# Optimization experiments

Measured on AMD Instinct MI355X. Metric: run time of the kernel, lower is better.

Reference implementation:

```python
import jax, jax.numpy as jnp
import numpy as np

ALPHA = 0.2  # LeakyReLU negative slope

def setup_inputs() -> dict:
    key = jax.random.key(0)
    k1, k2, k3, k4 = jax.random.split(key, 4)
    N, F_in, F_out = 8192, 512, 64
    x = jax.random.normal(k1, (N, F_in), dtype=jnp.float32)
    adj = jax.random.randint(k2, (N, N), 0, 2, dtype=jnp.int32)
    # xavier-normal-ish init
    weight = jax.random.normal(k3, (F_in, F_out), dtype=jnp.float32) * np.sqrt(2.0 / (F_in + F_out))
    a = jax.random.normal(k4, (2 * F_out, 1), dtype=jnp.float32) * np.sqrt(2.0 / (2 * F_out + 1))
    return {"x": x, "adj": adj, "weight": weight, "a": a}

def reference(x, adj, weight, a):
    # Wh: [N, F_out]
    Wh = x @ weight
    F_out = weight.shape[1]
    a1 = a[:F_out, 0]   # applies to source (row) node
    a2 = a[F_out:, 0]   # applies to target (col) node
    # e[i,j] = LeakyReLU(Wh[i]@a1 + Wh[j]@a2)  -- broadcast-add instead of O(N^2*2F) concat
    s1 = Wh @ a1        # [N]
    s2 = Wh @ a2        # [N]
    e = s1[:, None] + s2[None, :]              # [N, N]
    e = jnp.where(e > 0, e, ALPHA * e)         # LeakyReLU
    e = jnp.where(adj > 0, e, jnp.float32(-9e15))
    attention = jax.nn.softmax(e, axis=1)      # [N, N]
    h_prime = attention @ Wh                   # [N, F_out]
    return jax.nn.elu(h_prime)                 # concat=True -> ELU
```

## Files before the change

### kernel.cpp

```cpp
#include <hip/hip_runtime.h>
#include <hip/hip_bf16.h>
#include <cstdint>
#include <cstddef>

#define N_NODES 8192
#define F_IN 512
#define F_OUT 64
#define LOG2E 1.44269504f

#define JSPLIT 8
#define JPB (N_NODES / JSPLIT)
#define JC 256
#define NCHUNK (JPB / JC)

typedef __attribute__((ext_vector_type(8))) short short8v;
typedef __attribute__((ext_vector_type(4))) float f32x4;
typedef __attribute__((ext_vector_type(4))) int i32x4;
typedef __attribute__((ext_vector_type(4))) unsigned int u32x4;

static __device__ __forceinline__ unsigned short f2bf(float f) {
    union { float f; unsigned u; } v; v.f = f;
    unsigned u = v.u + 0x7FFFu + ((v.u >> 16) & 1u);
    return (unsigned short)(u >> 16);
}
static __device__ __forceinline__ float bf2f(unsigned short b) {
    union { unsigned u; float f; } v; v.u = ((unsigned)b) << 16;
    return v.f;
}
static __device__ __forceinline__ unsigned cvt_pk_bf16(float lo, float hi) {
    unsigned r;
    asm("v_cvt_pk_bf16_f32 %0, %1, %2" : "=v"(r) : "v"(lo), "v"(hi));
    return r;
}

__global__ __launch_bounds__(256)
void gat_wconv(const float* __restrict__ W, unsigned short* __restrict__ whf,
               unsigned short* __restrict__ wlf) {
    const int t = blockIdx.x * 256 + threadIdx.x;
    const int tile = t >> 6, lane = t & 63;
    const int kt = tile >> 2, ct = tile & 3;
    const int k0 = kt * 32 + ((lane >> 4) << 3);
    const int c  = ct * 16 + (lane & 15);
    short8v h, l;
    #pragma unroll
    for (int i = 0; i < 8; ++i) {
        float v = W[(size_t)(k0 + i) * F_OUT + c];
        unsigned short hb = f2bf(v);
        h[i] = (short)hb;
        l[i] = (short)f2bf(v - bf2f(hb));
    }
    const size_t dst = (size_t)tile * 512 + (size_t)lane * 8;
    *(short8v*)(whf + dst) = h;
    *(short8v*)(wlf + dst) = l;
}

__global__ __launch_bounds__(256)
void gat_prep(const float* __restrict__ x, const unsigned short* __restrict__ whf,
              const unsigned short* __restrict__ wlf, const float* __restrict__ a,
              unsigned short* __restrict__ whtf,
              float* __restrict__ s1, float* __restrict__ s2) {
    __shared__ f32x4 red[2][4][64];
    __shared__ unsigned short ldsT[64][40];
    const int tid = threadIdx.x;
    const int lane = tid & 63;
    const int wv = tid >> 6;
    const int rt = wv & 1;
    const int kh = wv >> 1;
    const int l15 = lane & 15, g = lane >> 4;
    const int jt = blockIdx.x;
    const int row0 = jt * 32 + rt * 16;

    f32x4 acc[4] = {{0.f,0.f,0.f,0.f},{0.f,0.f,0.f,0.f},{0.f,0.f,0.f,0.f},{0.f,0.f,0.f,0.f}};

    const float* xp = x + (size_t)(row0 + l15) * F_IN + kh * 256 + g * 8;
    float4 v[16];
    #pragma unroll
    for (int q = 0; q < 8; ++q) {
        v[2 * q]     = *(const float4*)(xp + q * 32);
        v[2 * q + 1] = *(const float4*)(xp + q * 32 + 4);
    }
    #pragma unroll
    for (int q = 0; q < 8; ++q) {
        const int kt = kh * 8 + q;
        float vv[8] = {v[2*q].x, v[2*q].y, v[2*q].z, v[2*q].w,
                       v[2*q+1].x, v[2*q+1].y, v[2*q+1].z, v[2*q+1].w};
        short8v xh, xl;
        #pragma unroll
        for (int i = 0; i < 8; ++i) {
            unsigned short hb = f2bf(vv[i]);
            xh[i] = (short)hb;
            xl[i] = (short)f2bf(vv[i] - bf2f(hb));
        }
        const unsigned short* wp = whf + (size_t)(kt * 4) * 512 + (size_t)lane * 8;
        const unsigned short* lp = wlf + (size_t)(kt * 4) * 512 + (size_t)lane * 8;
        #pragma unroll
        for (int ct = 0; ct < 4; ++ct) {
            short8v wh = *(const short8v*)(wp + ct * 512);
            short8v wl = *(const short8v*)(lp + ct * 512);
            acc[ct] = __builtin_amdgcn_mfma_f32_16x16x32_bf16(xh, wh, acc[ct], 0, 0, 0);
            acc[ct] = __builtin_amdgcn_mfma_f32_16x16x32_bf16(xl, wh, acc[ct], 0, 0, 0);
            acc[ct] = __builtin_amdgcn_mfma_f32_16x16x32_bf16(xh, wl, acc[ct], 0, 0, 0);
        }
    }

    if (kh == 1) {
        #pragma unroll
        for (int ct = 0; ct < 4; ++ct) red[rt][ct][lane] = acc[ct];
    }
    __syncthreads();

    if (kh == 0) {
        #pragma unroll
        for (int ct = 0; ct < 4; ++ct) acc[ct] += red[rt][ct][lane];

        #pragma unroll
        for (int r = 0; r < 4; ++r) {
            float p1 = 0.f, p2 = 0.f;
            #pragma unroll
            for (int ct = 0; ct < 4; ++ct) {
                p1 = fmaf(acc[ct][r], a[ct * 16 + l15], p1);
                p2 = fmaf(acc[ct][r], a[64 + ct * 16 + l15], p2);
            }
            p1 += __shfl_xor(p1, 1); p2 += __shfl_xor(p2, 1);
            p1 += __shfl_xor(p1, 2); p2 += __shfl_xor(p2, 2);
            p1 += __shfl_xor(p1, 4); p2 += __shfl_xor(p2, 4);
            p1 += __shfl_xor(p1, 8); p2 += __shfl_xor(p2, 8);
            if (l15 == 0) {
                s1[row0 + g * 4 + r] = p1 * LOG2E;
                s2[row0 + g * 4 + r] = p2 * LOG2E;
            }
        }

        #pragma unroll
        for (int ct = 0; ct < 4; ++ct) {
            ushort4 pk;
            pk.x = f2bf(acc[ct][0]); pk.y = f2bf(acc[ct][1]);
            pk.z = f2bf(acc[ct][2]); pk.w = f2bf(acc[ct][3]);
            *(ushort4*)&ldsT[ct * 16 + l15][rt * 16 + g * 4] = pk;
        }
    }
    __syncthreads();

    if (kh == 0) {
        #pragma unroll
        for (int fl = 0; fl < 2; ++fl) {
            const int ft = rt * 2 + fl;
            short8v sv = *(const short8v*)&ldsT[ft * 16 + l15][g * 8];
            *(short8v*)(whtf + ((size_t)jt * 4 + ft) * 512 + (size_t)lane * 8) = sv;
        }
    }
}

__global__ __launch_bounds__(512)
void gat_main(const int* __restrict__ adj, const unsigned short* __restrict__ whtf,
              const float* __restrict__ s1, const float* __restrict__ s2,
              float* __restrict__ numpart, float* __restrict__ denpart) {
    __shared__ unsigned short lds[2][JC * F_OUT];
    const int tid  = threadIdx.x;
    const int lane = tid & 63;
    const int wv   = tid >> 6;
    const int l15  = lane & 15, g = lane >> 4;
    const int rg   = blockIdx.x >> 3;
    const int js   = blockIdx.x & 7;
    const int rowbase = rg * 128 + wv * 16;
    const int row  = rowbase + l15;
    const int j0   = js * JPB;
    const float s1r = s1[row];

    const char* gbase = (const char*)whtf + (size_t)j0 * 128;
    const int*   aprow = adj + (size_t)row * N_NODES + j0 + g * 8;
    const float* s2b   = s2 + j0 + g * 8;

    f32x4 acc0 = {0.f, 0.f, 0.f, 0.f};
    f32x4 acc1 = acc0, acc2 = acc0, acc3 = acc0;
    float dsum = 0.f;

    #define STAGE(ch, buf) do { \
        const char* _g = gbase + (size_t)(ch) * 32768 + (size_t)tid * 16; \
        char* _l = (char*)&lds[buf][0] + (size_t)wv * 1024; \
        _Pragma("unroll") \
        for (int _i = 0; _i < 4; ++_i) \
            __builtin_amdgcn_global_load_lds( \
                (const __attribute__((address_space(1))) void*)(_g + _i * 8192), \
                (__attribute__((address_space(3))) void*)(_l + _i * 8192), 16, 0, 0); \
    } while (0)

    STAGE(0, 0);
    __syncthreads();

    for (int ch = 0; ch < NCHUNK; ++ch) {
        const int cur = ch & 1;
        if (ch < NCHUNK - 1) STAGE(ch + 1, cur ^ 1);

        const unsigned short* lbuf = &lds[cur][0];
        #pragma unroll
        for (int itg = 0; itg < 2; ++itg) {
            i32x4 aj[8];
            #pragma unroll
            for (int q = 0; q < 4; ++q) {
                const i32x4* ap = (const i32x4*)(aprow + ch * JC + itg * 128 + q * 32);
                aj[2 * q]     = ap[0];
                aj[2 * q + 1] = ap[1];
            }
            #pragma unroll
            for (int q = 0; q < 4; ++q) {
                const int it = itg * 4 + q;
                const int jw = ch * JC + it * 32;
                float4 sa = *(const float4*)(s2b + jw);
                float4 sb = *(const float4*)(s2b + jw + 4);

                short8v b0 = *(const short8v*)(lbuf + (it * 4 + 0) * 512 + lane * 8);
                short8v b1 = *(const short8v*)(lbuf + (it * 4 + 1) * 512 + lane * 8);
                short8v b2 = *(const short8v*)(lbuf + (it * 4 + 2) * 512 + lane * 8);
                short8v b3 = *(const short8v*)(lbuf + (it * 4 + 3) * 512 + lane * 8);

                float w0, w1, w2, w3, w4, w5, w6, w7;
                #define GAT_EL(wvar, ajv, s2v) do { \
                    float e = s1r + (s2v); e = fmaxf(e, 0.2f * e); \
                    float ex = __builtin_amdgcn_exp2f(e); \
                    wvar = ((ajv) > 0) ? ex : 0.f; dsum += wvar; } while (0);
                GAT_EL(w0, aj[2*q][0], sa.x) GAT_EL(w1, aj[2*q][1], sa.y)
                GAT_EL(w2, aj[2*q][2], sa.z) GAT_EL(w3, aj[2*q][3], sa.w)
                GAT_EL(w4, aj[2*q+1][0], sb.x) GAT_EL(w5, aj[2*q+1][1], sb.y)
                GAT_EL(w6, aj[2*q+1][2], sb.z) GAT_EL(w7, aj[2*q+1][3], sb.w)
                #undef GAT_EL

                u32x4 au;
                au[0] = cvt_pk_bf16(w0, w1);
                au[1] = cvt_pk_bf16(w2, w3);
                au[2] = cvt_pk_bf16(w4, w5);
                au[3] = cvt_pk_bf16(w6, w7);
                short8v afrag = __builtin_bit_cast(short8v, au);

                acc0 = __builtin_amdgcn_mfma_f32_16x16x32_bf16(afrag, b0, acc0, 0, 0, 0);
                acc1 = __builtin_amdgcn_mfma_f32_16x16x32_bf16(afrag, b1, acc1, 0, 0, 0);
                acc2 = __builtin_amdgcn_mfma_f32_16x16x32_bf16(afrag, b2, acc2, 0, 0, 0);
                acc3 = __builtin_amdgcn_mfma_f32_16x16x32_bf16(afrag, b3, acc3, 0, 0, 0);
            }
        }
        __syncthreads();
    }
    #undef STAGE

    dsum += __shfl_xor(dsum, 16);
    dsum += __shfl_xor(dsum, 32);
    if (lane < 16) denpart[(size_t)js * N_NODES + rowbase + lane] = dsum;

    float* np = numpart + ((size_t)js * N_NODES + rowbase) * F_OUT;
    #pragma unroll
    for (int r = 0; r < 4; ++r) {
        const int ro = (g * 4 + r) * F_OUT;
        np[ro +  0 + l15] = acc0[r];
        np[ro + 16 + l15] = acc1[r];
        np[ro + 32 + l15] = acc2[r];
        np[ro + 48 + l15] = acc3[r];
    }
}

__global__ __launch_bounds__(256)
void gat_combine(const float* __restrict__ numpart, const float* __restrict__ denpart,
                 float* __restrict__ out) {
    const int idx = blockIdx.x * 256 + threadIdx.x;
    const int r = idx >> 6;
    float num = 0.f, den = 0.f;
    #pragma unroll
    for (int c = 0; c < JSPLIT; ++c) {
        num += numpart[(size_t)c * N_NODES * F_OUT + idx];
        den += denpart[(size_t)c * N_NODES + r];
    }
    float h = num / den;
    out[idx] = h > 0.f ? h : __expf(h) - 1.f;
}

extern "C" void kernel_launch(void* const* d_in, const int* in_sizes, int n_in,
                              void* d_out, int out_size, void* d_ws, size_t ws_size,
                              hipStream_t stream) {
    const float* x      = (const float*)d_in[0];
    const int*   adj    = (const int*)d_in[1];
    const float* weight = (const float*)d_in[2];
    const float* a      = (const float*)d_in[3];
    float* out = (float*)d_out;

    char* ws = (char*)d_ws;
    unsigned short* whtf = (unsigned short*)ws;
    float* s1            = (float*)(ws + 1048576);
    float* s2            = (float*)(ws + 1048576 + 32768);
    unsigned short* whf  = (unsigned short*)(ws + 1048576 + 65536);
    unsigned short* wlf  = (unsigned short*)(ws + 1048576 + 131072);
    float* numpart       = (float*)(ws + 1048576 + 196608);
    float* denpart       = (float*)(ws + 1048576 + 196608 + (size_t)JSPLIT * N_NODES * F_OUT * 4);

    gat_wconv<<<16, 256, 0, stream>>>(weight, whf, wlf);
    gat_prep<<<N_NODES / 32, 256, 0, stream>>>(x, whf, wlf, a, whtf, s1, s2);
    gat_main<<<64 * JSPLIT, 512, 0, stream>>>(adj, whtf, s1, s2, numpart, denpart);
    gat_combine<<<N_NODES * F_OUT / 256, 256, 0, stream>>>(numpart, denpart, out);
}
```

Baseline: 85.97 us.

## Remap column-to-K assignment so each lane reads 32 contiguous adjacency ints

Changes which columns each lane group covers inside an MFMA K-slice, so every lane reads a contiguous 128-byte run of adj and s2 instead of strided 32-byte pieces. The Wh^T fragment layout written by the projection kernel is permuted to match, and all threads now take part in the store. It also adds a minimum-blocks hint to launch_bounds on the main kernel. The goal is better global-load coalescing and vector width on the dominant adjacency stream, with some risk of register pressure from the occupancy hint.

```diff
diff --git a/kernel.cpp b/kernel.cpp
--- a/kernel.cpp
+++ b/kernel.cpp
@@ -32,6 +32,7 @@
     asm("v_cvt_pk_bf16_f32 %0, %1, %2" : "=v"(r) : "v"(lo), "v"(hi));
     return r;
 }
+
 
 __global__ __launch_bounds__(256)
 void gat_wconv(const float* __restrict__ W, unsigned short* __restrict__ whf,
@@ -141,17 +142,18 @@
     }
     __syncthreads();
 
-    if (kh == 0) {
-        #pragma unroll
-        for (int fl = 0; fl < 2; ++fl) {
-            const int ft = rt * 2 + fl;
-            short8v sv = *(const short8v*)&ldsT[ft * 16 + l15][g * 8];
-            *(short8v*)(whtf + ((size_t)jt * 4 + ft) * 512 + (size_t)lane * 8) = sv;
-        }
-    }
-}
-
-__global__ __launch_bounds__(512)
+    {
+        const int jb = jt >> 2, gj = jt & 3;
+        const int m  = tid >> 6;
+        const int ct = (tid >> 4) & 3;
+        const int c  = tid & 15;
+        short8v sv = *(const short8v*)&ldsT[ct * 16 + c][m * 8];
+        *(short8v*)(whtf + (size_t)jb * 8192 + m * 2048 + ct * 512
+                         + (size_t)(gj * 16 + c) * 8) = sv;
+    }
+}
+
+__global__ __launch_bounds__(512, 4)
 void gat_main(const int* __restrict__ adj, const unsigned short* __restrict__ whtf,
               const float* __restrict__ s1, const float* __restrict__ s2,
               float* __restrict__ numpart, float* __restrict__ denpart) {
@@ -168,8 +170,8 @@
     const float s1r = s1[row];
 
     const char* gbase = (const char*)whtf + (size_t)j0 * 128;
-    const int*   aprow = adj + (size_t)row * N_NODES + j0 + g * 8;
-    const float* s2b   = s2 + j0 + g * 8;
+    const int*   abase = adj + (size_t)row * N_NODES + j0 + g * 32;
+    const float* s2base = s2 + j0 + g * 32;
 
     f32x4 acc0 = {0.f, 0.f, 0.f, 0.f};
     f32x4 acc1 = acc0, acc2 = acc0, acc3 = acc0;
@@ -194,35 +196,33 @@
 
         const unsigned short* lbuf = &lds[cur][0];
         #pragma unroll
-        for (int itg = 0; itg < 2; ++itg) {
+        for (int jb_l = 0; jb_l < 2; ++jb_l) {
+            const int jg = ch * JC + jb_l * 128;
             i32x4 aj[8];
             #pragma unroll
-            for (int q = 0; q < 4; ++q) {
-                const i32x4* ap = (const i32x4*)(aprow + ch * JC + itg * 128 + q * 32);
-                aj[2 * q]     = ap[0];
-                aj[2 * q + 1] = ap[1];
-            }
+            for (int q = 0; q < 8; ++q)
+                aj[q] = *(const i32x4*)(abase + jg + q * 4);
+
+            const unsigned short* gb = lbuf + jb_l * 8192;
             #pragma unroll
-            for (int q = 0; q < 4; ++q) {
-                const int it = itg * 4 + q;
-                const int jw = ch * JC + it * 32;
-                float4 sa = *(const float4*)(s2b + jw);
-                float4 sb = *(const float4*)(s2b + jw + 4);
-
-                short8v b0 = *(const short8v*)(lbuf + (it * 4 + 0) * 512 + lane * 8);
-                short8v b1 = *(const short8v*)(lbuf + (it * 4 + 1) * 512 + lane * 8);
-                short8v b2 = *(const short8v*)(lbuf + (it * 4 + 2) * 512 + lane * 8);
-                short8v b3 = *(const short8v*)(lbuf + (it * 4 + 3) * 512 + lane * 8);
+            for (int m = 0; m < 4; ++m) {
+                float4 sa = *(const float4*)(s2base + jg + m * 8);
+                float4 sb = *(const float4*)(s2base + jg + m * 8 + 4);
+
+                short8v b0 = *(const short8v*)(gb + m * 2048 +   0 + lane * 8);
+                short8v b1 = *(const short8v*)(gb + m * 2048 + 512 + lane * 8);
+                short8v b2 = *(const short8v*)(gb + m * 2048 + 1024 + lane * 8);
+                short8v b3 = *(const short8v*)(gb + m * 2048 + 1536 + lane * 8);
 
                 float w0, w1, w2, w3, w4, w5, w6, w7;
                 #define GAT_EL(wvar, ajv, s2v) do { \
                     float e = s1r + (s2v); e = fmaxf(e, 0.2f * e); \
                     float ex = __builtin_amdgcn_exp2f(e); \
                     wvar = ((ajv) > 0) ? ex : 0.f; dsum += wvar; } while (0);
-                GAT_EL(w0, aj[2*q][0], sa.x) GAT_EL(w1, aj[2*q][1], sa.y)
-                GAT_EL(w2, aj[2*q][2], sa.z) GAT_EL(w3, aj[2*q][3], sa.w)
-                GAT_EL(w4, aj[2*q+1][0], sb.x) GAT_EL(w5, aj[2*q+1][1], sb.y)
-                GAT_EL(w6, aj[2*q+1][2], sb.z) GAT_EL(w7, aj[2*q+1][3], sb.w)
+                GAT_EL(w0, aj[2*m][0], sa.x) GAT_EL(w1, aj[2*m][1], sa.y)
+                GAT_EL(w2, aj[2*m][2], sa.z) GAT_EL(w3, aj[2*m][3], sa.w)
+                GAT_EL(w4, aj[2*m+1][0], sb.x) GAT_EL(w5, aj[2*m+1][1], sb.y)
+                GAT_EL(w6, aj[2*m+1][2], sb.z) GAT_EL(w7, aj[2*m+1][3], sb.w)
                 #undef GAT_EL
 
                 u32x4 au;
```

Result: slower. 91.07 us (+5.9%).

## Load Wh B-fragments directly from global, drop LDS double buffering

Applied to the files above, without the earlier changes.

Removes the LDS staging of the pre-swizzled Wh tiles and the per-chunk barriers; each wave now reads its MFMA B fragments straight from global memory, which should mostly hit in L2 since every block reads the same data. Launch bounds now request 4 blocks per CU, so the freed LDS and tighter registers allow more resident waves. The cost is more global and L2 traffic for B operands that were previously shared across 8 waves through LDS, and higher load latency that the extra occupancy has to hide.

```diff
diff --git a/kernel.cpp b/kernel.cpp
--- a/kernel.cpp
+++ b/kernel.cpp
@@ -10,8 +10,6 @@
 
 #define JSPLIT 8
 #define JPB (N_NODES / JSPLIT)
-#define JC 256
-#define NCHUNK (JPB / JC)
 
 typedef __attribute__((ext_vector_type(8))) short short8v;
 typedef __attribute__((ext_vector_type(4))) float f32x4;
@@ -151,11 +149,10 @@
     }
 }
 
-__global__ __launch_bounds__(512)
+__global__ __launch_bounds__(512, 4)
 void gat_main(const int* __restrict__ adj, const unsigned short* __restrict__ whtf,
               const float* __restrict__ s1, const float* __restrict__ s2,
               float* __restrict__ numpart, float* __restrict__ denpart) {
-    __shared__ unsigned short lds[2][JC * F_OUT];
     const int tid  = threadIdx.x;
     const int lane = tid & 63;
     const int wv   = tid >> 6;
@@ -167,80 +164,58 @@
     const int j0   = js * JPB;
     const float s1r = s1[row];
 
-    const char* gbase = (const char*)whtf + (size_t)j0 * 128;
     const int*   aprow = adj + (size_t)row * N_NODES + j0 + g * 8;
     const float* s2b   = s2 + j0 + g * 8;
+    const unsigned short* bp = whtf + ((size_t)(j0 >> 5) * 4) * 512 + (size_t)lane * 8;
 
     f32x4 acc0 = {0.f, 0.f, 0.f, 0.f};
     f32x4 acc1 = acc0, acc2 = acc0, acc3 = acc0;
     float dsum = 0.f;
 
-    #define STAGE(ch, buf) do { \
-        const char* _g = gbase + (size_t)(ch) * 32768 + (size_t)tid * 16; \
-        char* _l = (char*)&lds[buf][0] + (size_t)wv * 1024; \
-        _Pragma("unroll") \
-        for (int _i = 0; _i < 4; ++_i) \
-            __builtin_amdgcn_global_load_lds( \
-                (const __attribute__((address_space(1))) void*)(_g + _i * 8192), \
-                (__attribute__((address_space(3))) void*)(_l + _i * 8192), 16, 0, 0); \
-    } while (0)
-
-    STAGE(0, 0);
-    __syncthreads();
-
-    for (int ch = 0; ch < NCHUNK; ++ch) {
-        const int cur = ch & 1;
-        if (ch < NCHUNK - 1) STAGE(ch + 1, cur ^ 1);
-
-        const unsigned short* lbuf = &lds[cur][0];
-        #pragma unroll
-        for (int itg = 0; itg < 2; ++itg) {
-            i32x4 aj[8];
-            #pragma unroll
-            for (int q = 0; q < 4; ++q) {
-                const i32x4* ap = (const i32x4*)(aprow + ch * JC + itg * 128 + q * 32);
-                aj[2 * q]     = ap[0];
-                aj[2 * q + 1] = ap[1];
-            }
-            #pragma unroll
-            for (int q = 0; q < 4; ++q) {
-                const int it = itg * 4 + q;
-                const int jw = ch * JC + it * 32;
-                float4 sa = *(const float4*)(s2b + jw);
-                float4 sb = *(const float4*)(s2b + jw + 4);
-
-                short8v b0 = *(const short8v*)(lbuf + (it * 4 + 0) * 512 + lane * 8);
-                short8v b1 = *(const short8v*)(lbuf + (it * 4 + 1) * 512 + lane * 8);
-                short8v b2 = *(const short8v*)(lbuf + (it * 4 + 2) * 512 + lane * 8);
-                short8v b3 = *(const short8v*)(lbuf + (it * 4 + 3) * 512 + lane * 8);
-
-                float w0, w1, w2, w3, w4, w5, w6, w7;
-                #define GAT_EL(wvar, ajv, s2v) do { \
-                    float e = s1r + (s2v); e = fmaxf(e, 0.2f * e); \
-                    float ex = __builtin_amdgcn_exp2f(e); \
-                    wvar = ((ajv) > 0) ? ex : 0.f; dsum += wvar; } while (0);
-                GAT_EL(w0, aj[2*q][0], sa.x) GAT_EL(w1, aj[2*q][1], sa.y)
-                GAT_EL(w2, aj[2*q][2], sa.z) GAT_EL(w3, aj[2*q][3], sa.w)
-                GAT_EL(w4, aj[2*q+1][0], sb.x) GAT_EL(w5, aj[2*q+1][1], sb.y)
-                GAT_EL(w6, aj[2*q+1][2], sb.z) GAT_EL(w7, aj[2*q+1][3], sb.w)
-                #undef GAT_EL
-
-                u32x4 au;
-                au[0] = cvt_pk_bf16(w0, w1);
-                au[1] = cvt_pk_bf16(w2, w3);
-                au[2] = cvt_pk_bf16(w4, w5);
-                au[3] = cvt_pk_bf16(w6, w7);
-                short8v afrag = __builtin_bit_cast(short8v, au);
-
-                acc0 = __builtin_amdgcn_mfma_f32_16x16x32_bf16(afrag, b0, acc0, 0, 0, 0);
-                acc1 = __builtin_amdgcn_mfma_f32_16x16x32_bf16(afrag, b1, acc1, 0, 0, 0);
-                acc2 = __builtin_amdgcn_mfma_f32_16x16x32_bf16(afrag, b2, acc2, 0, 0, 0);
-                acc3 = __builtin_amdgcn_mfma_f32_16x16x32_bf16(afrag, b3, acc3, 0, 0, 0);
-            }
-        }
-        __syncthreads();
-    }
-    #undef STAGE
+    for (int grp = 0; grp < JPB / 128; ++grp) {
+        i32x4 aj[8];
+        #pragma unroll
+        for (int q = 0; q < 4; ++q) {
+            const i32x4* ap = (const i32x4*)(aprow + grp * 128 + q * 32);
+            aj[2 * q]     = ap[0];
+            aj[2 * q + 1] = ap[1];
+        }
+        #pragma unroll
+        for (int q = 0; q < 4; ++q) {
+            const int jw = grp * 128 + q * 32;
+            float4 sa = *(const float4*)(s2b + jw);
+            float4 sb = *(const float4*)(s2b + jw + 4);
+
+            const unsigned short* bq = bp + (size_t)(grp * 4 + q) * 2048;
+            short8v b0 = *(const short8v*)(bq);
+            short8v b1 = *(const short8v*)(bq + 512);
+            short8v b2 = *(const short8v*)(bq + 1024);
+            short8v b3 = *(const short8v*)(bq + 1536);
+
+            float w0, w1, w2, w3, w4, w5, w6, w7;
+            #define GAT_EL(wvar, ajv, s2v) do { \
+                float e = s1r + (s2v); e = fmaxf(e, 0.2f * e); \
+                float ex = __builtin_amdgcn_exp2f(e); \
+                wvar = ((ajv) > 0) ? ex : 0.f; dsum += wvar; } while (0);
+            GAT_EL(w0, aj[2*q][0], sa.x) GAT_EL(w1, aj[2*q][1], sa.y)
+            GAT_EL(w2, aj[2*q][2], sa.z) GAT_EL(w3, aj[2*q][3], sa.w)
+            GAT_EL(w4, aj[2*q+1][0], sb.x) GAT_EL(w5, aj[2*q+1][1], sb.y)
+            GAT_EL(w6, aj[2*q+1][2], sb.z) GAT_EL(w7, aj[2*q+1][3], sb.w)
+            #undef GAT_EL
+
+            u32x4 au;
+            au[0] = cvt_pk_bf16(w0, w1);
+            au[1] = cvt_pk_bf16(w2, w3);
+            au[2] = cvt_pk_bf16(w4, w5);
+            au[3] = cvt_pk_bf16(w6, w7);
+            short8v afrag = __builtin_bit_cast(short8v, au);
+
+            acc0 = __builtin_amdgcn_mfma_f32_16x16x32_bf16(afrag, b0, acc0, 0, 0, 0);
+            acc1 = __builtin_amdgcn_mfma_f32_16x16x32_bf16(afrag, b1, acc1, 0, 0, 0);
+            acc2 = __builtin_amdgcn_mfma_f32_16x16x32_bf16(afrag, b2, acc2, 0, 0, 0);
+            acc3 = __builtin_amdgcn_mfma_f32_16x16x32_bf16(afrag, b3, acc3, 0, 0, 0);
+        }
+    }
 
     dsum += __shfl_xor(dsum, 16);
     dsum += __shfl_xor(dsum, 32);
```

Result: slower. 103.0 us (+19.8%).
